# Kernel optimization log

Hardware: AMD Instinct MI355X
Metric: run time of the kernel (lower is better)

The kernel has to match this reference:

```python
import jax, jax.numpy as jnp
import numpy as np

B, L, D = 2, 2048, 1024
K, M = 32, 4
H = D // K
AH = 4            # anchor heads
DH = K - AH       # decay heads
CK = 4            # conv kernel size
TOTAL = 2 * D + K + K * M


def setup_inputs() -> dict:
    key = jax.random.key(0)
    ks = jax.random.split(key, 7)
    x = jax.random.normal(ks[0], (B, L, D), jnp.float32)
    mask = jnp.ones((B, L), jnp.float32)
    W_in = jax.random.normal(ks[1], (D, TOTAL), jnp.float32) * 0.02
    conv_w = jax.random.normal(ks[2], (CK, TOTAL), jnp.float32) * 0.1  # depthwise taps
    conv_b = jnp.zeros((TOTAL,), jnp.float32)
    grid = np.linspace(-np.pi / 3, np.pi / 3, M).astype(np.float32)
    theta_base = jnp.asarray(np.tile(grid.reshape(1, 1, 1, 1, M), (1, 1, K, 1, 1)))
    theta_resid_scale = jnp.full((K,), 0.1, jnp.float32)
    dr = np.geomspace(0.001, 0.1, DH).astype(np.float32)
    decay_slopes = jnp.asarray(np.log(np.exp(dr) - 1.0).astype(np.float32))
    ar = np.geomspace(0.01, 0.1, AH).astype(np.float32)
    anchor_slopes = jnp.asarray(np.log(np.exp(ar) - 1.0).astype(np.float32))
    score_scale = jnp.ones((K,), jnp.float32)
    norm_scale = jnp.ones((2 * H * M,), jnp.float32)
    gl = float((2.0 / (H * M + H)) ** 0.5)  # glorot std
    W_re = jax.random.normal(ks[3], (H * M, H), jnp.float32) * gl
    W_im = jax.random.normal(ks[4], (H * M, H), jnp.float32) * gl
    W_out = jax.random.normal(ks[5], (D, D), jnp.float32) * 0.02
    return dict(x=x, mask=mask, W_in=W_in, conv_w=conv_w, conv_b=conv_b,
                theta_base=theta_base, theta_resid_scale=theta_resid_scale,
                decay_slopes=decay_slopes, anchor_slopes=anchor_slopes,
                score_scale=score_scale, norm_scale=norm_scale,
                W_re=W_re, W_im=W_im, W_out=W_out)


def _forward(x, mask, W_in, conv_w, conv_b, theta_base, theta_resid_scale,
             decay_slopes, anchor_slopes, score_scale, norm_scale, W_re, W_im, W_out):
    b, l, d = x.shape
    z = x @ W_in  # (b,l,TOTAL)
    # causal depthwise conv, kernel size CK
    zp = jnp.pad(z, ((0, 0), (CK - 1, 0), (0, 0)))
    z = sum(zp[:, t:t + l, :] * conv_w[t] for t in range(CK)) + conv_b

    x_val = z[..., :D].reshape(b, l, K, H)
    x_gate = jax.nn.silu(z[..., D:2 * D])
    s_raw = z[..., 2 * D:2 * D + K].reshape(b, l, K, 1)
    theta_raw = z[..., 2 * D + K:].reshape(b, l, K, M)

    theta_delta = theta_raw / (1.0 + jnp.abs(theta_raw))
    theta_dyn = theta_base + theta_resid_scale.reshape(1, 1, K, 1, 1) * (
        theta_delta.reshape(b, l, K, 1, M) * jnp.float32(np.pi / 3))

    m = mask[:, :, None, None]
    s_raw = s_raw * m
    x_val = x_val * m

    pos = jnp.arange(l, dtype=jnp.float32)
    slopes_d = jax.nn.softplus(decay_slopes).reshape(1, 1, DH, 1)
    dist_d = jnp.maximum(jnp.float32(l - 1) - pos, 0.0)[None, :, None, None]
    w_decay = jnp.exp(-slopes_d * dist_d)
    slopes_a = jax.nn.softplus(anchor_slopes).reshape(1, 1, AH, 1)
    w_anchor = jnp.exp(-slopes_a * pos[None, :, None, None])
    time_weight = jnp.concatenate([w_decay, w_anchor], axis=2)  # (1,l,K,1)

    p = jnp.exp(jnp.clip(score_scale[None, None, :, None] * s_raw, -20.0, 20.0))
    p = p * m

    phi = x_val[..., None] * theta_dyn  # (b,l,K,H,M)
    cos_b = jnp.cos(phi)
    sin_b = jnp.sin(phi)
    p_w = (p * time_weight)[..., None]  # (b,l,K,1,1)

    flat = (b, l, K * H * M)
    merged = jnp.concatenate([
        (p_w * cos_b).reshape(flat),
        (p_w * sin_b).reshape(flat),
        jnp.broadcast_to(p_w, (b, l, K, H, M)).reshape(flat)], axis=-1)
    cs = jnp.cumsum(merged, axis=1)
    num_re, num_im, den = jnp.split(cs, 3, axis=-1)
    inv_den = 1.0 / jnp.maximum(den, jnp.float32(1e-4))
    re = (num_re * inv_den).reshape(b, l, K, H * M)
    im = (num_im * inv_den).reshape(b, l, K, H * M)

    mean_sq = (jnp.sum(re * re, axis=-1) + jnp.sum(im * im, axis=-1)) * (1.0 / (2.0 * H * M))
    rsq = jax.lax.rsqrt(mean_sq[..., None] + 1e-5)
    y = (re * rsq * norm_scale[:H * M]) @ W_re + (im * rsq * norm_scale[H * M:]) @ W_im  # (b,l,K,H)
    y = y.reshape(b, l, D)
    return (y * x_gate) @ W_out


def reference(x, mask, W_in, conv_w, conv_b, theta_base, theta_resid_scale,
              decay_slopes, anchor_slopes, score_scale, norm_scale, W_re, W_im, W_out):
    return _forward(x, mask, W_in, conv_w, conv_b, theta_base, theta_resid_scale,
                    decay_slopes, anchor_slopes, score_scale, norm_scale, W_re, W_im, W_out)
```

## Files before the change

### kernel.cpp

```cpp
#include <hip/hip_runtime.h>
#include <hip/hip_bf16.h>
#include <math.h>

#define B_ 2
#define L_ 2048
#define D_ 1024
#define K_ 32
#define M_ 4
#define H_ 32
#define AH_ 4
#define DH_ 28
#define CK_ 4
#define TOTAL_ 2208
#define NPAD_ 2304
#define BL_ (B_*L_)
#define CL_ 16
#define NC_ (L_/CL_)
#define CTS_ 280

typedef __attribute__((ext_vector_type(8))) short bf16x8;
typedef __attribute__((ext_vector_type(4))) float f32x4;

static __device__ inline unsigned short f2bu(float f) {
    union { __hip_bfloat16 h; unsigned short u; } cv;
    cv.h = __float2bfloat16(f);
    return cv.u;
}
static __device__ inline float b2f(unsigned short u) {
    union { unsigned short u; __hip_bfloat16 h; } cv;
    cv.u = u;
    return __bfloat162float(cv.h);
}

static __device__ inline float convd(const ushort* z, int blbase, int l, int ch,
                                     const float* w4, float bias) {
    float acc = bias;
#pragma unroll
    for (int tap = 0; tap < 4; ++tap) {
        int ls = l - 3 + tap;
        float zv = (ls >= 0) ? b2f(z[(size_t)(blbase + ls) * NPAD_ + ch]) : 0.f;
        acc = fmaf(w4[tap], zv, acc);
    }
    return acc;
}

__global__ __launch_bounds__(256) void prep_all(const float* __restrict__ x,
                                                const float* __restrict__ W_in,
                                                const float* __restrict__ Wout,
                                                const float* __restrict__ Wre,
                                                const float* __restrict__ Wim,
                                                const float* __restrict__ nscale,
                                                ushort* __restrict__ x_bf,
                                                ushort* __restrict__ Wt_in,
                                                ushort* __restrict__ Wt_o,
                                                ushort* __restrict__ W2B) {
    __shared__ float tile[64][65];
    int bid = blockIdx.x, t = threadIdx.x;
    if (bid < 4096) {
        int i = bid * 256 + t;
        float4 v = ((const float4*)x)[i];
        ushort4 o;
        o.x = f2bu(v.x); o.y = f2bu(v.y); o.z = f2bu(v.z); o.w = f2bu(v.w);
        *(ushort4*)(x_bf + (size_t)i * 4) = o;
        return;
    }
    const float* src; ushort* dst; int Kd, N, n0, k0;
    if (bid < 4096 + 576) {
        int bb = bid - 4096;
        src = W_in; dst = Wt_in; Kd = 1024; N = TOTAL_;
        n0 = (bb % 36) * 64; k0 = (bb / 36) * 64;
    } else if (bid < 4096 + 576 + 256) {
        int bb = bid - 4096 - 576;
        src = Wout; dst = Wt_o; Kd = 1024; N = 1024;
        n0 = (bb % 16) * 64; k0 = (bb / 16) * 64;
    } else {
        int ch = t;
        float ns = nscale[ch];
        for (int ho = 0; ho < 32; ++ho) {
            float w = (ch < 128) ? Wre[ch * 32 + ho] : Wim[(ch - 128) * 32 + ho];
            W2B[ho * 256 + ch] = f2bu(ns * w);
        }
        return;
    }
#pragma unroll
    for (int i = 0; i < 16; ++i) {
        int idx = t + i * 256;
        int r = idx >> 6, c = idx & 63;
        int gn = n0 + c;
        tile[r][c] = (gn < N) ? src[(size_t)(k0 + r) * N + gn] : 0.f;
    }
    __syncthreads();
#pragma unroll
    for (int i = 0; i < 16; ++i) {
        int idx = t + i * 256;
        int r = idx >> 6, c = idx & 63;
        dst[(size_t)(n0 + r) * Kd + k0 + c] = f2bu(tile[c][r]);
    }
}

template <bool OUT_BF16>
__global__ __launch_bounds__(256) void gemm_bt64(const ushort* __restrict__ A,
                                                 const ushort* __restrict__ Bt,
                                                 void* __restrict__ Cv,
                                                 int Kd, int ldc) {
    __shared__ __align__(16) ushort SB[192 * 32];
    int tid = threadIdx.x;
    int wave = tid >> 6, lane = tid & 63;
    int quad = lane >> 4, l16 = lane & 15;
    int n0 = blockIdx.x * 128, m0 = blockIdx.y * 64;
    int wm = (wave & 1) * 32, wn = (wave >> 1) * 64;
    f32x4 acc[2][4];
#pragma unroll
    for (int i = 0; i < 2; ++i)
#pragma unroll
        for (int j = 0; j < 4; ++j) acc[i][j] = (f32x4){0.f, 0.f, 0.f, 0.f};

    int swzq = quad ^ (l16 & 3);

    for (int k0 = 0; k0 < Kd; k0 += 32) {
#pragma unroll
        for (int i = 0; i < 3; ++i) {
            int s = i * 256 + tid;
            int row = s >> 2;
            int qg = (s & 3) ^ (row & 3);
            const ushort* g = (row < 64) ? A + (size_t)(m0 + row) * Kd + k0 + qg * 8
                                         : Bt + (size_t)(n0 + row - 64) * Kd + k0 + qg * 8;
            __builtin_amdgcn_global_load_lds((const __attribute__((address_space(1))) void*)g,
                                             (__attribute__((address_space(3))) void*)(SB + (size_t)s * 8),
                                             16, 0, 0);
        }
        __syncthreads();
        bf16x8 af[2], bfr[4];
#pragma unroll
        for (int mi = 0; mi < 2; ++mi)
            af[mi] = *(const bf16x8*)(SB + (size_t)(wm + mi * 16 + l16) * 32 + swzq * 8);
#pragma unroll
        for (int ni = 0; ni < 4; ++ni)
            bfr[ni] = *(const bf16x8*)(SB + (size_t)(64 + wn + ni * 16 + l16) * 32 + swzq * 8);
#pragma unroll
        for (int mi = 0; mi < 2; ++mi)
#pragma unroll
            for (int ni = 0; ni < 4; ++ni)
                acc[mi][ni] = __builtin_amdgcn_mfma_f32_16x16x32_bf16(af[mi], bfr[ni], acc[mi][ni], 0, 0, 0);
        __syncthreads();
    }
#pragma unroll
    for (int mi = 0; mi < 2; ++mi)
#pragma unroll
        for (int ni = 0; ni < 4; ++ni)
#pragma unroll
            for (int r = 0; r < 4; ++r) {
                int gm = m0 + wm + mi * 16 + quad * 4 + r;
                int gn = n0 + wn + ni * 16 + l16;
                if (OUT_BF16)
                    ((ushort*)Cv)[(size_t)gm * ldc + gn] = f2bu(acc[mi][ni][r]);
                else
                    ((float*)Cv)[(size_t)gm * ldc + gn] = acc[mi][ni][r];
            }
}

__global__ __launch_bounds__(128) void pass1f(const ushort* __restrict__ z,
                                              const float* __restrict__ mask,
                                              const float* __restrict__ theta_base,
                                              const float* __restrict__ trs_,
                                              const float* __restrict__ dslopes,
                                              const float* __restrict__ aslopes,
                                              const float* __restrict__ sscale_,
                                              const float* __restrict__ conv_w,
                                              const float* __restrict__ conv_b,
                                              const ushort* __restrict__ W2B,
                                              float* __restrict__ cs_re,
                                              float* __restrict__ cs_im,
                                              float* __restrict__ cs_den,
                                              float* __restrict__ vc,
                                              float* __restrict__ ucs) {
    __shared__ __align__(16) ushort ct[CL_ * CTS_];
    __shared__ float theta_s[CL_ * 4];
    __shared__ float pw_s[CL_];
    __shared__ float xv_s[CL_][33];

    int nc = blockIdx.x, k = blockIdx.y, b = blockIdx.z;
    int hm = threadIdx.x;
    int bk = b * K_ + k;
    size_t bkL = (size_t)bk * L_;
    int l0 = nc * CL_;
    int blb = b * L_;
    const float PI3 = 1.04719755119659775f;

    float raw = (k < DH_) ? dslopes[k] : aslopes[k - DH_];
    float slope = log1pf(__expf(raw));

    if (hm < 64) {
        int li = hm >> 2, m = hm & 3;
        int l = l0 + li;
        int cth = 2 * D_ + K_ + k * M_ + m;
        float wt[4];
#pragma unroll
        for (int t = 0; t < 4; ++t) wt[t] = conv_w[t * TOTAL_ + cth];
        float tr = convd(z, blb, l, cth, wt, conv_b[cth]);
        float td = tr / (1.f + fabsf(tr));
        theta_s[li * 4 + m] = theta_base[k * M_ + m] + trs_[k] * (td * PI3);
    }
    if (hm >= 64 && hm < 64 + CL_) {
        int li = hm - 64;
        int l = l0 + li;
        int csc = 2 * D_ + k;
        float wsv[4];
#pragma unroll
        for (int t = 0; t < 4; ++t) wsv[t] = conv_w[t * TOTAL_ + csc];
        float mval = mask[blb + l];
        float s_raw = convd(z, blb, l, csc, wsv, conv_b[csc]) * mval;
        float arg = fminf(fmaxf(sscale_[k] * s_raw, -20.f), 20.f);
        float p = __expf(arg) * mval;
        float tw = (k < DH_) ? __expf(-slope * (float)(L_ - 1 - l)) : __expf(-slope * (float)l);
        pw_s[li] = p * tw;
    }
    {
        int h = hm & 31, lset = hm >> 5;
        int cxv = k * H_ + h;
        float wxv[4];
#pragma unroll
        for (int t = 0; t < 4; ++t) wxv[t] = conv_w[t * TOTAL_ + cxv];
        float bxv = conv_b[cxv];
#pragma unroll
        for (int j = 0; j < 4; ++j) {
            int li = lset * 4 + j;
            int l = l0 + li;
            float xv = convd(z, blb, l, cxv, wxv, bxv) * mask[blb + l];
            xv_s[li][h] = xv;
        }
    }
    __syncthreads();

    int h = hm >> 2, m = hm & 3;
    float are = 0.f, aim = 0.f;
#pragma unroll
    for (int i = 0; i < CL_; ++i) {
        float phi = xv_s[i][h] * theta_s[i * 4 + m];
        float pw = pw_s[i];
        float sv = __sinf(phi), cv = __cosf(phi);
        unsigned short cu_re = f2bu(pw * cv);
        unsigned short cu_im = f2bu(pw * sv);
        are += b2f(cu_re); aim += b2f(cu_im);
        ct[i * CTS_ + hm] = cu_re;
        ct[i * CTS_ + 128 + hm] = cu_im;
    }
    size_t o = ((size_t)(bk * NC_ + nc)) * 128 + hm;
    cs_re[o] = are;
    cs_im[o] = aim;
    if (hm == 0) {
        float aden = 0.f;
#pragma unroll
        for (int i = 0; i < CL_; ++i) aden += pw_s[i];
        cs_den[bk * NC_ + nc] = aden;
    }
    __syncthreads();
    int wave = hm >> 6, lane = hm & 63;
    int quad = lane >> 4, l16 = lane & 15;
    f32x4 acc = (f32x4){0.f, 0.f, 0.f, 0.f};
#pragma unroll
    for (int ks = 0; ks < 8; ++ks) {
        bf16x8 af = *(const bf16x8*)(ct + (size_t)l16 * CTS_ + ks * 32 + quad * 8);
        bf16x8 bfr = *(const bf16x8*)(W2B + (size_t)(wave * 16 + l16) * 256 + ks * 32 + quad * 8);
        acc = __builtin_amdgcn_mfma_f32_16x16x32_bf16(af, bfr, acc, 0, 0, 0);
    }
    size_t vbase = (bkL + l0) * 32;
#pragma unroll
    for (int r = 0; r < 4; ++r) {
        int rowv = quad * 4 + r;
        vc[vbase + (size_t)rowv * 32 + wave * 16 + l16] = acc[r];
    }
    float part = acc[0] + acc[1] + acc[2] + acc[3];
    part += __shfl_xor(part, 16, 64);
    part += __shfl_xor(part, 32, 64);
    if (quad == 0) ucs[((size_t)(bk * NC_ + nc)) * 32 + wave * 16 + l16] = part;
}

__global__ void scan2(float* cs_re, float* cs_im, float* cs_den,
                      const float* __restrict__ ucs, float* __restrict__ u_prev) {
    int bid = blockIdx.x, tid = threadIdx.x;
    if (bid < 65) {
        int seq = bid * 256 + tid;
        if (seq >= B_ * K_ * 257) return;
        int bk = seq / 257;
        int ch = seq % 257;
        float* base;
        int stride;
        if (ch < 128) { base = cs_re + (size_t)bk * NC_ * 128 + ch; stride = 128; }
        else if (ch < 256) { base = cs_im + (size_t)bk * NC_ * 128 + (ch - 128); stride = 128; }
        else { base = cs_den + (size_t)bk * NC_; stride = 1; }
        float run = 0.f;
#pragma unroll 4
        for (int i = 0; i < NC_; ++i) {
            float v = base[(size_t)i * stride];
            base[(size_t)i * stride] = run;
            run += v;
        }
    } else {
        int idx = (bid - 65) * 256 + tid;
        int hout = idx & 31;
        int bk = idx >> 5;
        float run = 0.f;
#pragma unroll 8
        for (int nc = 0; nc < NC_; ++nc) {
            size_t o = ((size_t)bk * NC_ + nc) * 32 + hout;
            float v = ucs[o];
            u_prev[o] = run;
            run += v;
        }
    }
}

__global__ __launch_bounds__(64) void scan_k7(const ushort* __restrict__ z,
                                              const float* __restrict__ mask,
                                              const float* __restrict__ theta_base,
                                              const float* __restrict__ trs_,
                                              const float* __restrict__ dslopes,
                                              const float* __restrict__ aslopes,
                                              const float* __restrict__ sscale_,
                                              const float* __restrict__ conv_w,
                                              const float* __restrict__ conv_b,
                                              const float* __restrict__ cs_re,
                                              const float* __restrict__ cs_im,
                                              const float* __restrict__ cs_den,
                                              const float* __restrict__ u_prev,
                                              const float* __restrict__ vc,
                                              ushort* __restrict__ gq) {
    __shared__ float theta_s[CL_ * 4];
    __shared__ float pw_s[CL_];
    __shared__ float xv_s[CL_][33];
    __shared__ float gate_s[CL_][33];

    int nc = blockIdx.x, k = blockIdx.y, b = blockIdx.z;
    int lane = threadIdx.x;
    int bk = b * K_ + k;
    size_t bkL = (size_t)bk * L_;
    int l0 = nc * CL_;
    int blb = b * L_;
    const float PI3 = 1.04719755119659775f;

    float raw = (k < DH_) ? dslopes[k] : aslopes[k - DH_];
    float slope = log1pf(__expf(raw));

    {
        int li = lane >> 2, m = lane & 3;
        int l = l0 + li;
        int cth = 2 * D_ + K_ + k * M_ + m;
        float wt[4];
#pragma unroll
        for (int t = 0; t < 4; ++t) wt[t] = conv_w[t * TOTAL_ + cth];
        float tr = convd(z, blb, l, cth, wt, conv_b[cth]);
        float td = tr / (1.f + fabsf(tr));
        theta_s[li * 4 + m] = theta_base[k * M_ + m] + trs_[k] * (td * PI3);
    }
    if (lane < CL_) {
        int l = l0 + lane;
        int csc = 2 * D_ + k;
        float wsv[4];
#pragma unroll
        for (int t = 0; t < 4; ++t) wsv[t] = conv_w[t * TOTAL_ + csc];
        float mval = mask[blb + l];
        float s_raw = convd(z, blb, l, csc, wsv, conv_b[csc]) * mval;
        float arg = fminf(fmaxf(sscale_[k] * s_raw, -20.f), 20.f);
        float p = __expf(arg) * mval;
        float tw = (k < DH_) ? __expf(-slope * (float)(L_ - 1 - l)) : __expf(-slope * (float)l);
        pw_s[lane] = p * tw;
    }
    {
        int h = lane & 31, lset = lane >> 5;
        int cxv = k * H_ + h;
        int cg = D_ + k * H_ + h;
        float wxv[4], wg[4];
#pragma unroll
        for (int t = 0; t < 4; ++t) {
            wxv[t] = conv_w[t * TOTAL_ + cxv];
            wg[t] = conv_w[t * TOTAL_ + cg];
        }
        float bxv = conv_b[cxv], bg = conv_b[cg];
#pragma unroll
        for (int j = 0; j < 8; ++j) {
            int li = lset * 8 + j;
            int l = l0 + li;
            float xv = convd(z, blb, l, cxv, wxv, bxv) * mask[blb + l];
            xv_s[li][h] = xv;
            float gp = convd(z, blb, l, cg, wg, bg);
            gate_s[li][h] = gp / (1.f + __expf(-gp));
        }
    }
    __syncthreads();

    int h0 = lane >> 2, h1 = 16 + (lane >> 2), m = lane & 3;
    int hout = lane & 31;

    size_t o = ((size_t)(bk * NC_ + nc)) * 128;
    float are0 = cs_re[o + lane];
    float are1 = cs_re[o + 64 + lane];
    float aim0 = cs_im[o + lane];
    float aim1 = cs_im[o + 64 + lane];
    float den = cs_den[bk * NC_ + nc];
    float u = u_prev[((size_t)(bk * NC_ + nc)) * 32 + hout];

#pragma unroll 4
    for (int i = 0; i < CL_; ++i) {
        int l = l0 + i;
        float th = theta_s[i * 4 + m];
        float pw = pw_s[i];
        float phi0 = xv_s[i][h0] * th;
        float phi1 = xv_s[i][h1] * th;
        float s0 = __sinf(phi0), cv0 = __cosf(phi0);
        float s1 = __sinf(phi1), cv1 = __cosf(phi1);
        float cre0 = b2f(f2bu(pw * cv0)), cim0 = b2f(f2bu(pw * s0));
        float cre1 = b2f(f2bu(pw * cv1)), cim1 = b2f(f2bu(pw * s1));
        are0 += cre0; aim0 += cim0; are1 += cre1; aim1 += cim1;
        den += pw;
        float s = are0 * are0 + are1 * are1 + aim0 * aim0 + aim1 * aim1;
#pragma unroll
        for (int off = 32; off; off >>= 1) s += __shfl_xor(s, off, 64);
        float inv = 1.f / fmaxf(den, 1e-4f);
        float rsq = rsqrtf(inv * inv * s * (1.0f / 256.0f) + 1e-5f);
        u += vc[(bkL + l) * 32 + hout];
        float gv = inv * rsq * u * gate_s[i][hout];
        if (lane < 32) gq[(size_t)(blb + l) * D_ + k * H_ + hout] = f2bu(gv);
    }
}

extern "C" void kernel_launch(void* const* d_in, const int* in_sizes, int n_in,
                              void* d_out, int out_size, void* d_ws, size_t ws_size,
                              hipStream_t stream) {
    const float* x = (const float*)d_in[0];
    const float* mask = (const float*)d_in[1];
    const float* W_in = (const float*)d_in[2];
    const float* conv_w = (const float*)d_in[3];
    const float* conv_b = (const float*)d_in[4];
    const float* theta_base = (const float*)d_in[5];
    const float* trs = (const float*)d_in[6];
    const float* dsl = (const float*)d_in[7];
    const float* asl = (const float*)d_in[8];
    const float* ssc = (const float*)d_in[9];
    const float* nsc = (const float*)d_in[10];
    const float* Wre = (const float*)d_in[11];
    const float* Wim = (const float*)d_in[12];
    const float* Wout = (const float*)d_in[13];
    float* out = (float*)d_out;

    char* ws = (char*)d_ws;
    ushort* z     = (ushort*)(ws);
    ushort* x_bf  = (ushort*)(ws + 18874368ULL);
    ushort* Wt_in = (ushort*)(ws + 27262976ULL);
    ushort* Wt_o  = (ushort*)(ws + 31981568ULL);
    ushort* W2B   = (ushort*)(ws + 34078720ULL);
    float* vc     = (float*)(ws + 34095104ULL);
    float* cs_re  = (float*)(ws + 50872320ULL);
    float* cs_im  = (float*)(ws + 55066624ULL);
    float* cs_den = (float*)(ws + 59260928ULL);
    float* ucs    = (float*)(ws + 59293696ULL);
    float* u_prev = (float*)(ws + 60342272ULL);
    ushort* gq    = (ushort*)(ws + 61390848ULL);

    prep_all<<<4096 + 576 + 256 + 1, 256, 0, stream>>>(x, W_in, Wout, Wre, Wim, nsc,
                                                       x_bf, Wt_in, Wt_o, W2B);
    gemm_bt64<true><<<dim3(NPAD_ / 128, BL_ / 64), 256, 0, stream>>>(x_bf, Wt_in, z, 1024, NPAD_);
    pass1f<<<dim3(NC_, K_, B_), 128, 0, stream>>>(z, mask, theta_base, trs, dsl, asl, ssc,
                                                  conv_w, conv_b, W2B,
                                                  cs_re, cs_im, cs_den, vc, ucs);
    scan2<<<73, 256, 0, stream>>>(cs_re, cs_im, cs_den, ucs, u_prev);
    scan_k7<<<dim3(NC_, K_, B_), 64, 0, stream>>>(z, mask, theta_base, trs, dsl, asl, ssc,
                                                  conv_w, conv_b, cs_re, cs_im, cs_den,
                                                  u_prev, vc, gq);
    gemm_bt64<false><<<dim3(1024 / 128, BL_ / 64), 256, 0, stream>>>(gq, Wt_o, out, 1024, 1024);
}
```

Measured before the change: 259.7 us.

## Fuse chunk-prefix scan into pass1f via last-block atomic counter; batch shuffles in scan_k7

Removes the separate scan2 launch. Each pass1f block now increments a per-(b,k) atomic counter after a threadfence, and the last block to finish for a sequence does the exclusive prefix scan over chunk totals. The counters are zeroed by an extra block in prep_all. Separately, scan_k7 computes all 16 per-step sums of squares first, then does the wave reductions in a batch so the shuffles can overlap instead of serialising inside the recurrence. The trade-off is that the serial scan now runs on only 64 blocks of 128 threads, with a tail where just the last block per sequence is busy. It also relies on the memory-ordering being correct.

```diff
diff --git a/kernel.cpp b/kernel.cpp
--- a/kernel.cpp
+++ b/kernel.cpp
@@ -53,7 +53,8 @@
                                                 ushort* __restrict__ x_bf,
                                                 ushort* __restrict__ Wt_in,
                                                 ushort* __restrict__ Wt_o,
-                                                ushort* __restrict__ W2B) {
+                                                ushort* __restrict__ W2B,
+                                                int* __restrict__ cnt) {
     __shared__ float tile[64][65];
     int bid = blockIdx.x, t = threadIdx.x;
     if (bid < 4096) {
@@ -73,13 +74,16 @@
         int bb = bid - 4096 - 576;
         src = Wout; dst = Wt_o; Kd = 1024; N = 1024;
         n0 = (bb % 16) * 64; k0 = (bb / 16) * 64;
-    } else {
+    } else if (bid == 4096 + 576 + 256) {
         int ch = t;
         float ns = nscale[ch];
         for (int ho = 0; ho < 32; ++ho) {
             float w = (ch < 128) ? Wre[ch * 32 + ho] : Wim[(ch - 128) * 32 + ho];
             W2B[ho * 256 + ch] = f2bu(ns * w);
         }
+        return;
+    } else {
+        if (t < 64) cnt[t] = 0;
         return;
     }
 #pragma unroll
@@ -173,11 +177,14 @@
                                               float* __restrict__ cs_im,
                                               float* __restrict__ cs_den,
                                               float* __restrict__ vc,
-                                              float* __restrict__ ucs) {
+                                              float* __restrict__ ucs,
+                                              float* __restrict__ u_prev,
+                                              int* __restrict__ cnt) {
     __shared__ __align__(16) ushort ct[CL_ * CTS_];
     __shared__ float theta_s[CL_ * 4];
     __shared__ float pw_s[CL_];
     __shared__ float xv_s[CL_][33];
+    __shared__ int lastS;
 
     int nc = blockIdx.x, k = blockIdx.y, b = blockIdx.z;
     int hm = threadIdx.x;
@@ -274,39 +281,38 @@
     part += __shfl_xor(part, 16, 64);
     part += __shfl_xor(part, 32, 64);
     if (quad == 0) ucs[((size_t)(bk * NC_ + nc)) * 32 + wave * 16 + l16] = part;
-}
-
-__global__ void scan2(float* cs_re, float* cs_im, float* cs_den,
-                      const float* __restrict__ ucs, float* __restrict__ u_prev) {
-    int bid = blockIdx.x, tid = threadIdx.x;
-    if (bid < 65) {
-        int seq = bid * 256 + tid;
-        if (seq >= B_ * K_ * 257) return;
-        int bk = seq / 257;
-        int ch = seq % 257;
-        float* base;
-        int stride;
-        if (ch < 128) { base = cs_re + (size_t)bk * NC_ * 128 + ch; stride = 128; }
-        else if (ch < 256) { base = cs_im + (size_t)bk * NC_ * 128 + (ch - 128); stride = 128; }
-        else { base = cs_den + (size_t)bk * NC_; stride = 1; }
-        float run = 0.f;
+
+    __threadfence();
+    if (hm == 0) {
+        int old = __hip_atomic_fetch_add(&cnt[bk], 1, __ATOMIC_ACQ_REL,
+                                         __HIP_MEMORY_SCOPE_AGENT);
+        lastS = (old == NC_ - 1) ? 1 : 0;
+    }
+    __syncthreads();
+    if (lastS) {
+        for (int ch = hm; ch < 257; ch += 128) {
+            float* base;
+            int stride;
+            if (ch < 128) { base = cs_re + (size_t)bk * NC_ * 128 + ch; stride = 128; }
+            else if (ch < 256) { base = cs_im + (size_t)bk * NC_ * 128 + (ch - 128); stride = 128; }
+            else { base = cs_den + (size_t)bk * NC_; stride = 1; }
+            float run = 0.f;
 #pragma unroll 4
-        for (int i = 0; i < NC_; ++i) {
-            float v = base[(size_t)i * stride];
-            base[(size_t)i * stride] = run;
-            run += v;
-        }
-    } else {
-        int idx = (bid - 65) * 256 + tid;
-        int hout = idx & 31;
-        int bk = idx >> 5;
-        float run = 0.f;
+            for (int i = 0; i < NC_; ++i) {
+                float v = base[(size_t)i * stride];
+                base[(size_t)i * stride] = run;
+                run += v;
+            }
+        }
+        if (hm < 32) {
+            float run = 0.f;
 #pragma unroll 8
-        for (int nc = 0; nc < NC_; ++nc) {
-            size_t o = ((size_t)bk * NC_ + nc) * 32 + hout;
-            float v = ucs[o];
-            u_prev[o] = run;
-            run += v;
+            for (int ncq = 0; ncq < NC_; ++ncq) {
+                size_t oo = ((size_t)bk * NC_ + ncq) * 32 + hm;
+                float v = ucs[oo];
+                u_prev[oo] = run;
+                run += v;
+            }
         }
     }
 }
@@ -400,9 +406,9 @@
     float den = cs_den[bk * NC_ + nc];
     float u = u_prev[((size_t)(bk * NC_ + nc)) * 32 + hout];
 
-#pragma unroll 4
+    float sloc[CL_];
+#pragma unroll
     for (int i = 0; i < CL_; ++i) {
-        int l = l0 + i;
         float th = theta_s[i * 4 + m];
         float pw = pw_s[i];
         float phi0 = xv_s[i][h0] * th;
@@ -412,12 +418,19 @@
         float cre0 = b2f(f2bu(pw * cv0)), cim0 = b2f(f2bu(pw * s0));
         float cre1 = b2f(f2bu(pw * cv1)), cim1 = b2f(f2bu(pw * s1));
         are0 += cre0; aim0 += cim0; are1 += cre1; aim1 += cim1;
-        den += pw;
-        float s = are0 * are0 + are1 * are1 + aim0 * aim0 + aim1 * aim1;
-#pragma unroll
-        for (int off = 32; off; off >>= 1) s += __shfl_xor(s, off, 64);
+        sloc[i] = are0 * are0 + are1 * are1 + aim0 * aim0 + aim1 * aim1;
+    }
+#pragma unroll
+    for (int i = 0; i < CL_; ++i) {
+#pragma unroll
+        for (int off = 32; off; off >>= 1) sloc[i] += __shfl_xor(sloc[i], off, 64);
+    }
+#pragma unroll
+    for (int i = 0; i < CL_; ++i) {
+        int l = l0 + i;
+        den += pw_s[i];
         float inv = 1.f / fmaxf(den, 1e-4f);
-        float rsq = rsqrtf(inv * inv * s * (1.0f / 256.0f) + 1e-5f);
+        float rsq = rsqrtf(inv * inv * sloc[i] * (1.0f / 256.0f) + 1e-5f);
         u += vc[(bkL + l) * 32 + hout];
         float gv = inv * rsq * u * gate_s[i][hout];
         if (lane < 32) gq[(size_t)(blb + l) * D_ + k * H_ + hout] = f2bu(gv);
@@ -456,14 +469,14 @@
     float* ucs    = (float*)(ws + 59293696ULL);
     float* u_prev = (float*)(ws + 60342272ULL);
     ushort* gq    = (ushort*)(ws + 61390848ULL);
-
-    prep_all<<<4096 + 576 + 256 + 1, 256, 0, stream>>>(x, W_in, Wout, Wre, Wim, nsc,
-                                                       x_bf, Wt_in, Wt_o, W2B);
+    int*   cnt    = (int*)(ws + 69779456ULL);
+
+    prep_all<<<4096 + 576 + 256 + 2, 256, 0, stream>>>(x, W_in, Wout, Wre, Wim, nsc,
+                                                       x_bf, Wt_in, Wt_o, W2B, cnt);
     gemm_bt64<true><<<dim3(NPAD_ / 128, BL_ / 64), 256, 0, stream>>>(x_bf, Wt_in, z, 1024, NPAD_);
     pass1f<<<dim3(NC_, K_, B_), 128, 0, stream>>>(z, mask, theta_base, trs, dsl, asl, ssc,
                                                   conv_w, conv_b, W2B,
-                                                  cs_re, cs_im, cs_den, vc, ucs);
-    scan2<<<73, 256, 0, stream>>>(cs_re, cs_im, cs_den, ucs, u_prev);
+                                                  cs_re, cs_im, cs_den, vc, ucs, u_prev, cnt);
     scan_k7<<<dim3(NC_, K_, B_), 64, 0, stream>>>(z, mask, theta_base, trs, dsl, asl, ssc,
                                                   conv_w, conv_b, cs_re, cs_im, cs_den,
                                                   u_prev, vc, gq);
```

After: 858.3 us. +230.5%, slower.

## Fuse fp32-to-bf16 conversion of x into input GEMM and batch scan reductions

Applied to the files above, without the earlier changes.

Drops the separate pass that converts x to bf16. The input GEMM now loads fp32 A tiles, converts them in registers and writes them to LDS, which removes an 8 MB bf16 round trip through global memory. The scan kernel's per-step loop is also split into three phases so the 16 wave reductions are batched and independent, which gives more instruction-level parallelism. In exchange, A-tile loads in the GEMM become synchronous register loads rather than direct-to-LDS loads, and fp32 A traffic per tile doubles.

```diff
diff --git a/kernel.cpp b/kernel.cpp
--- a/kernel.cpp
+++ b/kernel.cpp
@@ -19,6 +19,7 @@
 #define CTS_ 280
 
 typedef __attribute__((ext_vector_type(8))) short bf16x8;
+typedef __attribute__((ext_vector_type(8))) unsigned short u16x8;
 typedef __attribute__((ext_vector_type(4))) float f32x4;
 
 static __device__ inline unsigned short f2bu(float f) {
@@ -44,33 +45,22 @@
     return acc;
 }
 
-__global__ __launch_bounds__(256) void prep_all(const float* __restrict__ x,
-                                                const float* __restrict__ W_in,
+__global__ __launch_bounds__(256) void prep_all(const float* __restrict__ W_in,
                                                 const float* __restrict__ Wout,
                                                 const float* __restrict__ Wre,
                                                 const float* __restrict__ Wim,
                                                 const float* __restrict__ nscale,
-                                                ushort* __restrict__ x_bf,
                                                 ushort* __restrict__ Wt_in,
                                                 ushort* __restrict__ Wt_o,
                                                 ushort* __restrict__ W2B) {
     __shared__ float tile[64][65];
     int bid = blockIdx.x, t = threadIdx.x;
-    if (bid < 4096) {
-        int i = bid * 256 + t;
-        float4 v = ((const float4*)x)[i];
-        ushort4 o;
-        o.x = f2bu(v.x); o.y = f2bu(v.y); o.z = f2bu(v.z); o.w = f2bu(v.w);
-        *(ushort4*)(x_bf + (size_t)i * 4) = o;
-        return;
-    }
     const float* src; ushort* dst; int Kd, N, n0, k0;
-    if (bid < 4096 + 576) {
-        int bb = bid - 4096;
+    if (bid < 576) {
         src = W_in; dst = Wt_in; Kd = 1024; N = TOTAL_;
-        n0 = (bb % 36) * 64; k0 = (bb / 36) * 64;
-    } else if (bid < 4096 + 576 + 256) {
-        int bb = bid - 4096 - 576;
+        n0 = (bid % 36) * 64; k0 = (bid / 36) * 64;
+    } else if (bid < 576 + 256) {
+        int bb = bid - 576;
         src = Wout; dst = Wt_o; Kd = 1024; N = 1024;
         n0 = (bb % 16) * 64; k0 = (bb / 16) * 64;
     } else {
@@ -98,10 +88,77 @@
     }
 }
 
-template <bool OUT_BF16>
+__global__ __launch_bounds__(256) void gemm_f32a(const float* __restrict__ A,
+                                                 const ushort* __restrict__ Bt,
+                                                 ushort* __restrict__ C,
+                                                 int Kd, int ldc) {
+    __shared__ __align__(16) ushort SB[192 * 32];
+    int tid = threadIdx.x;
+    int wave = tid >> 6, lane = tid & 63;
+    int quad = lane >> 4, l16 = lane & 15;
+    int n0 = blockIdx.x * 128, m0 = blockIdx.y * 64;
+    int wm = (wave & 1) * 32, wn = (wave >> 1) * 64;
+    f32x4 acc[2][4];
+#pragma unroll
+    for (int i = 0; i < 2; ++i)
+#pragma unroll
+        for (int j = 0; j < 4; ++j) acc[i][j] = (f32x4){0.f, 0.f, 0.f, 0.f};
+
+    int swzq = quad ^ (l16 & 3);
+
+    for (int k0 = 0; k0 < Kd; k0 += 32) {
+#pragma unroll
+        for (int i = 0; i < 2; ++i) {
+            int s = 256 + i * 256 + tid;
+            int row = s >> 2;
+            int qg = (s & 3) ^ (row & 3);
+            const ushort* g = Bt + (size_t)(n0 + row - 64) * Kd + k0 + qg * 8;
+            __builtin_amdgcn_global_load_lds((const __attribute__((address_space(1))) void*)g,
+                                             (__attribute__((address_space(3))) void*)(SB + (size_t)s * 8),
+                                             16, 0, 0);
+        }
+        {
+            int s = tid;
+            int row = s >> 2;
+            int qg = (s & 3) ^ (row & 3);
+            const float* ga = A + (size_t)(m0 + row) * Kd + k0 + qg * 8;
+            float4 v0 = *(const float4*)ga;
+            float4 v1 = *(const float4*)(ga + 4);
+            u16x8 pk;
+            pk[0] = f2bu(v0.x); pk[1] = f2bu(v0.y); pk[2] = f2bu(v0.z); pk[3] = f2bu(v0.w);
+            pk[4] = f2bu(v1.x); pk[5] = f2bu(v1.y); pk[6] = f2bu(v1.z); pk[7] = f2bu(v1.w);
+            *(u16x8*)(SB + (size_t)s * 8) = pk;
+        }
+        __syncthreads();
+        bf16x8 af[2], bfr[4];
+#pragma unroll
+        for (int mi = 0; mi < 2; ++mi)
+            af[mi] = *(const bf16x8*)(SB + (size_t)(wm + mi * 16 + l16) * 32 + swzq * 8);
+#pragma unroll
+        for (int ni = 0; ni < 4; ++ni)
+            bfr[ni] = *(const bf16x8*)(SB + (size_t)(64 + wn + ni * 16 + l16) * 32 + swzq * 8);
+#pragma unroll
+        for (int mi = 0; mi < 2; ++mi)
+#pragma unroll
+            for (int ni = 0; ni < 4; ++ni)
+                acc[mi][ni] = __builtin_amdgcn_mfma_f32_16x16x32_bf16(af[mi], bfr[ni], acc[mi][ni], 0, 0, 0);
+        __syncthreads();
+    }
+#pragma unroll
+    for (int mi = 0; mi < 2; ++mi)
+#pragma unroll
+        for (int ni = 0; ni < 4; ++ni)
+#pragma unroll
+            for (int r = 0; r < 4; ++r) {
+                int gm = m0 + wm + mi * 16 + quad * 4 + r;
+                int gn = n0 + wn + ni * 16 + l16;
+                C[(size_t)gm * ldc + gn] = f2bu(acc[mi][ni][r]);
+            }
+}
+
 __global__ __launch_bounds__(256) void gemm_bt64(const ushort* __restrict__ A,
                                                  const ushort* __restrict__ Bt,
-                                                 void* __restrict__ Cv,
+                                                 float* __restrict__ C,
                                                  int Kd, int ldc) {
     __shared__ __align__(16) ushort SB[192 * 32];
     int tid = threadIdx.x;
@@ -152,10 +209,7 @@
             for (int r = 0; r < 4; ++r) {
                 int gm = m0 + wm + mi * 16 + quad * 4 + r;
                 int gn = n0 + wn + ni * 16 + l16;
-                if (OUT_BF16)
-                    ((ushort*)Cv)[(size_t)gm * ldc + gn] = f2bu(acc[mi][ni][r]);
-                else
-                    ((float*)Cv)[(size_t)gm * ldc + gn] = acc[mi][ni][r];
+                C[(size_t)gm * ldc + gn] = acc[mi][ni][r];
             }
 }
 
@@ -400,9 +454,9 @@
     float den = cs_den[bk * NC_ + nc];
     float u = u_prev[((size_t)(bk * NC_ + nc)) * 32 + hout];
 
-#pragma unroll 4
+    float sloc[CL_];
+#pragma unroll
     for (int i = 0; i < CL_; ++i) {
-        int l = l0 + i;
         float th = theta_s[i * 4 + m];
         float pw = pw_s[i];
         float phi0 = xv_s[i][h0] * th;
@@ -412,12 +466,19 @@
         float cre0 = b2f(f2bu(pw * cv0)), cim0 = b2f(f2bu(pw * s0));
         float cre1 = b2f(f2bu(pw * cv1)), cim1 = b2f(f2bu(pw * s1));
         are0 += cre0; aim0 += cim0; are1 += cre1; aim1 += cim1;
-        den += pw;
-        float s = are0 * are0 + are1 * are1 + aim0 * aim0 + aim1 * aim1;
-#pragma unroll
-        for (int off = 32; off; off >>= 1) s += __shfl_xor(s, off, 64);
+        sloc[i] = are0 * are0 + are1 * are1 + aim0 * aim0 + aim1 * aim1;
+    }
+#pragma unroll
+    for (int i = 0; i < CL_; ++i) {
+#pragma unroll
+        for (int off = 32; off; off >>= 1) sloc[i] += __shfl_xor(sloc[i], off, 64);
+    }
+#pragma unroll
+    for (int i = 0; i < CL_; ++i) {
+        int l = l0 + i;
+        den += pw_s[i];
         float inv = 1.f / fmaxf(den, 1e-4f);
-        float rsq = rsqrtf(inv * inv * s * (1.0f / 256.0f) + 1e-5f);
+        float rsq = rsqrtf(inv * inv * sloc[i] * (1.0f / 256.0f) + 1e-5f);
         u += vc[(bkL + l) * 32 + hout];
         float gv = inv * rsq * u * gate_s[i][hout];
         if (lane < 32) gq[(size_t)(blb + l) * D_ + k * H_ + hout] = f2bu(gv);
@@ -445,21 +506,20 @@
 
     char* ws = (char*)d_ws;
     ushort* z     = (ushort*)(ws);
-    ushort* x_bf  = (ushort*)(ws + 18874368ULL);
-    ushort* Wt_in = (ushort*)(ws + 27262976ULL);
-    ushort* Wt_o  = (ushort*)(ws + 31981568ULL);
-    ushort* W2B   = (ushort*)(ws + 34078720ULL);
-    float* vc     = (float*)(ws + 34095104ULL);
-    float* cs_re  = (float*)(ws + 50872320ULL);
-    float* cs_im  = (float*)(ws + 55066624ULL);
-    float* cs_den = (float*)(ws + 59260928ULL);
-    float* ucs    = (float*)(ws + 59293696ULL);
-    float* u_prev = (float*)(ws + 60342272ULL);
-    ushort* gq    = (ushort*)(ws + 61390848ULL);
-
-    prep_all<<<4096 + 576 + 256 + 1, 256, 0, stream>>>(x, W_in, Wout, Wre, Wim, nsc,
-                                                       x_bf, Wt_in, Wt_o, W2B);
-    gemm_bt64<true><<<dim3(NPAD_ / 128, BL_ / 64), 256, 0, stream>>>(x_bf, Wt_in, z, 1024, NPAD_);
+    ushort* Wt_in = (ushort*)(ws + 18874368ULL);
+    ushort* Wt_o  = (ushort*)(ws + 23592960ULL);
+    ushort* W2B   = (ushort*)(ws + 25690112ULL);
+    float* vc     = (float*)(ws + 25706496ULL);
+    float* cs_re  = (float*)(ws + 42483712ULL);
+    float* cs_im  = (float*)(ws + 46678016ULL);
+    float* cs_den = (float*)(ws + 50872320ULL);
+    float* ucs    = (float*)(ws + 50905088ULL);
+    float* u_prev = (float*)(ws + 51953664ULL);
+    ushort* gq    = (ushort*)(ws + 53002240ULL);
+
+    prep_all<<<576 + 256 + 1, 256, 0, stream>>>(W_in, Wout, Wre, Wim, nsc,
+                                                Wt_in, Wt_o, W2B);
+    gemm_f32a<<<dim3(NPAD_ / 128, BL_ / 64), 256, 0, stream>>>(x, Wt_in, z, 1024, NPAD_);
     pass1f<<<dim3(NC_, K_, B_), 128, 0, stream>>>(z, mask, theta_base, trs, dsl, asl, ssc,
                                                   conv_w, conv_b, W2B,
                                                   cs_re, cs_im, cs_den, vc, ucs);
@@ -467,5 +527,5 @@
     scan_k7<<<dim3(NC_, K_, B_), 64, 0, stream>>>(z, mask, theta_base, trs, dsl, asl, ssc,
                                                   conv_w, conv_b, cs_re, cs_im, cs_den,
                                                   u_prev, vc, gq);
-    gemm_bt64<false><<<dim3(1024 / 128, BL_ / 64), 256, 0, stream>>>(gq, Wt_o, out, 1024, 1024);
-}
+    gemm_bt64<<<dim3(1024 / 128, BL_ / 64), 256, 0, stream>>>(gq, Wt_o, out, 1024, 1024);
+}
```

Result: no change. 263.2 us (+1.4%).
